# Kernel tuning notes

Measured on AMD Instinct MI355X. Metric: run time of the kernel, lower is better.

Reference implementation:

```python
import jax, jax.numpy as jnp
import numpy as np

BLOCK = 32      # BFP block size along contraction axis
MBITS = 8       # signed mantissa bits shared-exponent format


def bfp_quant(x):
    """Block-floating-point quantize along the last axis.

    Each contiguous block of BLOCK elements shares an exponent taken from the
    block max; mantissas are MBITS-bit signed integers, round-to-nearest.
    Returns the dequantized (reconstructed) float32 tensor.
    """
    *lead, n = x.shape
    xb = x.reshape(*lead, n // BLOCK, BLOCK)
    maxabs = jnp.max(jnp.abs(xb), axis=-1, keepdims=True)
    # shared exponent per block; guard zero blocks
    e = jnp.floor(jnp.log2(jnp.maximum(maxabs, jnp.float32(1e-38))))
    step = jnp.exp2(e - (MBITS - 1))            # quantization step 2^(e-m+1)
    qmax = 2 ** (MBITS - 1) - 1
    q = jnp.clip(jnp.round(xb / step), -qmax - 1, qmax)
    out = jnp.where(maxabs > 0, q * step, jnp.float32(0.0))
    return out.reshape(x.shape)


def setup_inputs() -> dict:
    key = jax.random.key(0)
    k1, k2 = jax.random.split(key)
    lhs_mat = jax.random.normal(k1, (1, 16, 4096, 64), dtype=jnp.float32)
    rhs_mat = jax.random.normal(k2, (1, 16, 64, 4096), dtype=jnp.float32)
    return {"lhs_mat": lhs_mat, "rhs_mat": rhs_mat}


def reference(lhs_mat, rhs_mat):
    # custom_transpose_4d(rhs) -> rhs_t [B,H,N,K]; then BFP GEMM quantizes both
    # operands along their last axis (the contraction axis K) and multiplies.
    rhs_t = jnp.swapaxes(rhs_mat, -1, -2)
    lhs_q = bfp_quant(lhs_mat)   # [B,H,M,K]
    rhs_q = bfp_quant(rhs_t)     # [B,H,N,K]
    return jnp.einsum('bhmk,bhnk->bhmn', lhs_q, rhs_q)
```

## Files before the change

### kernel.cpp

```cpp
#include <hip/hip_runtime.h>
#include <hip/hip_bf16.h>
#include <stdint.h>


#define BH 16
#define MDIM 4096
#define NDIM 4096
#define KDIM 64

typedef __bf16 bf16x8 __attribute__((ext_vector_type(8)));
typedef float f32x16 __attribute__((ext_vector_type(16)));

__device__ __forceinline__ float bfp_quant_val(float x, float maxabs) {
  int e = (int)(__float_as_uint(fmaxf(maxabs, 1e-38f)) >> 23) - 127;
  e = e < -119 ? -119 : e;
  float rstep = __int_as_float((134 - e) << 23);
  float step  = __int_as_float((e + 120) << 23);
  float q = rintf(x * rstep);
  q = fminf(127.0f, fmaxf(-128.0f, q));
  return (maxabs > 0.0f) ? q * step : 0.0f;
}

__device__ __forceinline__ unsigned short f32_to_bf16_exact(float r) {
  return (unsigned short)(__float_as_uint(r) >> 16);
}

__global__ __launch_bounds__(256) void quant_lhs_kernel(
    const float* __restrict__ in, unsigned short* __restrict__ out) {
  int tid = threadIdx.x;
  int lane = tid & 63;
  size_t row = (size_t)blockIdx.x * 4 + (tid >> 6);
  size_t idx = row * KDIM + lane;
  float x = in[idx];
  float v = fabsf(x);
#pragma unroll
  for (int off = 1; off < 32; off <<= 1)
    v = fmaxf(v, __shfl_xor(v, off));
  out[idx] = f32_to_bf16_exact(bfp_quant_val(x, v));
}

__global__ __launch_bounds__(256) void quant_rhs_kernel(
    const float* __restrict__ in, unsigned short* __restrict__ out) {
  int h = blockIdx.y;
  int n = blockIdx.x * 256 + threadIdx.x;
  const float* src = in + (size_t)h * KDIM * NDIM + n;
  float x[KDIM];
#pragma unroll
  for (int k = 0; k < KDIM; ++k) x[k] = src[(size_t)k * NDIM];
  float ma0 = 0.0f, ma1 = 0.0f;
#pragma unroll
  for (int k = 0; k < 32; ++k) ma0 = fmaxf(ma0, fabsf(x[k]));
#pragma unroll
  for (int k = 32; k < 64; ++k) ma1 = fmaxf(ma1, fabsf(x[k]));
  unsigned short* dst = out + ((size_t)h * NDIM + n) * KDIM;
#pragma unroll
  for (int g = 0; g < 8; ++g) {
    union { unsigned short us[8]; uint4 v; } pk;
#pragma unroll
    for (int i = 0; i < 8; ++i) {
      int k = g * 8 + i;
      pk.us[i] = f32_to_bf16_exact(bfp_quant_val(x[k], (k < 32) ? ma0 : ma1));
    }
    ((uint4*)dst)[g] = pk.v;
  }
}

__global__ __launch_bounds__(256) void gemm_kernel(
    const unsigned short* __restrict__ aq, const unsigned short* __restrict__ bq,
    float* __restrict__ c) {
  const int h = blockIdx.z;
  const int m0 = blockIdx.x * 128;
  const int n0 = blockIdx.y * 128;
  const int wave = threadIdx.x >> 6;
  const int lane = threadIdx.x & 63;
  const int l31 = lane & 31;
  const int kb = (lane >> 5) * 8;
  const int mBase = m0 + wave * 32;

  const unsigned short* arow = aq + ((size_t)(h * MDIM + mBase + l31) * KDIM + kb);
  const unsigned short* brow = bq + ((size_t)(h * NDIM + n0 + l31) * KDIM + kb);

  f32x16 acc[4] = {};

#pragma unroll
  for (int s = 0; s < 4; ++s) {
    uint4 au = *(const uint4*)(arow + s * 16);
    bf16x8 af = __builtin_bit_cast(bf16x8, au);
#pragma unroll
    for (int j = 0; j < 4; ++j) {
      uint4 bu = *(const uint4*)(brow + (size_t)j * 32 * KDIM + s * 16);
      bf16x8 bfr = __builtin_bit_cast(bf16x8, bu);
      acc[j] = __builtin_amdgcn_mfma_f32_32x32x16_bf16(af, bfr, acc[j], 0, 0, 0);
    }
  }

  float* cbase = c + (size_t)h * MDIM * NDIM;
#pragma unroll
  for (int j = 0; j < 4; ++j) {
    int n = n0 + j * 32 + l31;
#pragma unroll
    for (int r = 0; r < 16; ++r) {
      int row = (r & 3) + 8 * (r >> 2) + 4 * (lane >> 5);
      cbase[(size_t)(mBase + row) * NDIM + n] = acc[j][r];
    }
  }
}

extern "C" void kernel_launch(void* const* d_in, const int* in_sizes, int n_in,
                              void* d_out, int out_size, void* d_ws, size_t ws_size,
                              hipStream_t stream) {
  const float* lhs = (const float*)d_in[0];
  const float* rhs = (const float*)d_in[1];
  float* out = (float*)d_out;

  unsigned short* aq = (unsigned short*)d_ws;
  unsigned short* bq = aq + (size_t)BH * MDIM * KDIM;

  quant_lhs_kernel<<<dim3(BH * MDIM / 4), 256, 0, stream>>>(lhs, aq);
  quant_rhs_kernel<<<dim3(NDIM / 256, BH), 256, 0, stream>>>(rhs, bq);
  gemm_kernel<<<dim3(MDIM / 128, NDIM / 128, BH), 256, 0, stream>>>(aq, bq, out);
}
```

Measured before the change: 1.128 ms.

## Stage GEMM operands and output tile through LDS with XCD-aware block remap

```diff
diff --git a/kernel.cpp b/kernel.cpp
--- a/kernel.cpp
+++ b/kernel.cpp
@@ -1,5 +1,4 @@
 #include <hip/hip_runtime.h>
-#include <hip/hip_bf16.h>
 #include <stdint.h>
 
 
@@ -10,6 +9,7 @@
 
 typedef __bf16 bf16x8 __attribute__((ext_vector_type(8)));
 typedef float f32x16 __attribute__((ext_vector_type(16)));
+typedef float f32x4 __attribute__((ext_vector_type(4)));
 
 __device__ __forceinline__ float bfp_quant_val(float x, float maxabs) {
   int e = (int)(__float_as_uint(fmaxf(maxabs, 1e-38f)) >> 23) - 127;
@@ -68,41 +68,77 @@
 __global__ __launch_bounds__(256) void gemm_kernel(
     const unsigned short* __restrict__ aq, const unsigned short* __restrict__ bq,
     float* __restrict__ c) {
-  const int h = blockIdx.z;
-  const int m0 = blockIdx.x * 128;
-  const int n0 = blockIdx.y * 128;
-  const int wave = threadIdx.x >> 6;
-  const int lane = threadIdx.x & 63;
-  const int l31 = lane & 31;
-  const int kb = (lane >> 5) * 8;
-  const int mBase = m0 + wave * 32;
+  __shared__ __align__(16) char smem[32768];
 
-  const unsigned short* arow = aq + ((size_t)(h * MDIM + mBase + l31) * KDIM + kb);
-  const unsigned short* brow = bq + ((size_t)(h * NDIM + n0 + l31) * KDIM + kb);
+  int wg = (int)blockIdx.x;
+  wg = (wg & 7) * 2048 + (wg >> 3);
+  const int h  = wg >> 10;
+  const int bx = wg & 31;
+  const int by = (wg >> 5) & 31;
+  const int m0 = bx * 128;
+  const int n0 = by * 128;
+
+  const int tid  = threadIdx.x;
+  const int wave = tid >> 6;
+  const int lane = tid & 63;
+  const int l31  = lane & 31;
+  const int hi   = lane >> 5;
+
+  const unsigned short* abase = aq + (size_t)(h * MDIM + m0) * KDIM;
+  const unsigned short* bbase = bq + (size_t)(h * NDIM + n0) * KDIM;
+#pragma unroll
+  for (int it = 0; it < 8; ++it) {
+    int ci    = it * 256 + tid;
+    int local = ci & 1023;
+    int row   = local >> 3;
+    int p     = local & 7;
+    int cl    = p ^ (row & 7);
+    const unsigned short* src =
+        ((ci < 1024) ? abase + (size_t)row * KDIM
+                     : bbase + (size_t)row * KDIM) + cl * 8;
+    uint4 v = *(const uint4*)src;
+    *(uint4*)(smem + ci * 16) = v;
+  }
+  __syncthreads();
+
+  const int xo = l31 & 7;
+  const char* As = smem + (wave * 32 + l31) * 128;
+  const char* Bs = smem + 16384 + l31 * 128;
 
   f32x16 acc[4] = {};
-
 #pragma unroll
   for (int s = 0; s < 4; ++s) {
-    uint4 au = *(const uint4*)(arow + s * 16);
-    bf16x8 af = __builtin_bit_cast(bf16x8, au);
+    const int co = ((hi + 2 * s) ^ xo) << 4;
+    bf16x8 af = *(const bf16x8*)(As + co);
 #pragma unroll
     for (int j = 0; j < 4; ++j) {
-      uint4 bu = *(const uint4*)(brow + (size_t)j * 32 * KDIM + s * 16);
-      bf16x8 bfr = __builtin_bit_cast(bf16x8, bu);
+      bf16x8 bfr = *(const bf16x8*)(Bs + j * 4096 + co);
       acc[j] = __builtin_amdgcn_mfma_f32_32x32x16_bf16(af, bfr, acc[j], 0, 0, 0);
     }
   }
+  __syncthreads();
 
-  float* cbase = c + (size_t)h * MDIM * NDIM;
+  float* cslice = (float*)(smem + wave * 8192);
+  float* cbase  = c + (size_t)h * MDIM * NDIM;
 #pragma unroll
-  for (int j = 0; j < 4; ++j) {
-    int n = n0 + j * 32 + l31;
+  for (int pass = 0; pass < 2; ++pass) {
 #pragma unroll
-    for (int r = 0; r < 16; ++r) {
-      int row = (r & 3) + 8 * (r >> 2) + 4 * (lane >> 5);
-      cbase[(size_t)(mBase + row) * NDIM + n] = acc[j][r];
+    for (int j = 0; j < 4; ++j) {
+#pragma unroll
+      for (int rr = 0; rr < 8; ++rr) {
+        int r = pass * 8 + rr;
+        int lrow = (r & 3) + 8 * (r >> 2) + 4 * hi - pass * 16;
+        cslice[lrow * 128 + j * 32 + l31] = acc[j][r];
+      }
     }
+#pragma unroll
+    for (int it = 0; it < 8; ++it) {
+      int lrow = it * 2 + hi;
+      f32x4 v = *(const f32x4*)(cslice + lrow * 128 + l31 * 4);
+      size_t grow = (size_t)(m0 + wave * 32 + pass * 16 + lrow);
+      *(f32x4*)(cbase + grow * NDIM + n0 + l31 * 4) = v;
+    }
+    asm volatile("s_waitcnt lgkmcnt(0)" ::: "memory");
   }
 }
 
@@ -118,5 +154,5 @@
 
   quant_lhs_kernel<<<dim3(BH * MDIM / 4), 256, 0, stream>>>(lhs, aq);
   quant_rhs_kernel<<<dim3(NDIM / 256, BH), 256, 0, stream>>>(rhs, bq);
-  gemm_kernel<<<dim3(MDIM / 128, NDIM / 128, BH), 256, 0, stream>>>(aq, bq, out);
+  gemm_kernel<<<dim3(MDIM / 128 * NDIM / 128 * BH), 256, 0, stream>>>(aq, bq, out);
 }
```

Result: faster. 1.065 ms (-5.6%).
